# Kernel optimization log

Hardware: AMD Instinct MI355X
Metric: run time of the kernel (lower is better)

Reference implementation:

```python
import math
import jax, jax.numpy as jnp
import numpy as np

NEG = -1e32
H = 8          # n_heads
L2 = 1e-05


def _ln(x, g, b):
    m = jnp.mean(x, -1, keepdims=True)
    v = jnp.mean((x - m) ** 2, -1, keepdims=True)
    return g * (x - m) * jax.lax.rsqrt(v + 1e-5) + b


def _attn(q, k, v, gam, mask_k, zero_pad):
    # q,k,v: [B,H,S,d]; monotonic distance-decay attention (AKT style)
    d_k = q.shape[-1]
    S = q.shape[2]
    scores = jnp.einsum('bhqd,bhkd->bhqk', q, k) / math.sqrt(d_k)
    # torch: triu(ones, k=mask)==0  ->  tril(0) if mask_k==1 else tril(-1)
    mask = jnp.tril(jnp.ones((S, S), bool), 0 if mask_k == 1 else -1)[None, None]
    # first (detached) softmax, used only to build the distance effect
    s_ = jax.nn.softmax(jnp.where(mask, scores, NEG), -1) * mask
    distcum = jnp.cumsum(s_, -1)
    disttot = jnp.sum(s_, -1, keepdims=True)
    idx = jnp.arange(S, dtype=jnp.float32)
    pos = jnp.abs(idx[None, :] - idx[:, None])[None, None]  # |j - i|
    dist = jax.lax.stop_gradient(
        jnp.sqrt(jnp.clip((disttot - distcum) * pos, 0.0, None)))
    gamma = -jax.nn.softplus(gam)[None]  # [1,H,1,1], gam is learned
    total_effect = jnp.clip(jnp.exp(dist * gamma), 1e-5, 1e5)
    scores = jax.nn.softmax(jnp.where(mask, scores * total_effect, NEG), -1)
    if zero_pad:
        scores = scores.at[:, :, 0, :].set(0.0)
    return jnp.einsum('bhqk,bhkd->bhqd', scores, v)


def _mha(qi, ki, vi, kW, kb, vW, vb, oW, ob, gam, mask_k, zero_pad):
    # kq_same=True: q and k both use k_linear
    B, S = qi.shape[:2]
    sp = lambda x: x.reshape(B, S, H, -1).transpose(0, 2, 1, 3)
    q = sp(qi @ kW + kb)
    k = sp(ki @ kW + kb)
    v = sp(vi @ vW + vb)
    o = _attn(q, k, v, gam, mask_k, zero_pad)
    o = o.transpose(0, 2, 1, 3).reshape(B, S, -1)
    return o @ oW + ob


def _tlayer(query, key, values, mask_k, zero_pad, apply_pos,
            kW, kb, vW, vb, oW, ob, gam, ln1g, ln1b,
            f1W, f1b, f2W, f2b, ln2g, ln2b):
    q2 = _mha(query, key, values, kW, kb, vW, vb, oW, ob, gam, mask_k, zero_pad)
    x = _ln(query + q2, ln1g, ln1b)
    if apply_pos:
        ff = jax.nn.relu(x @ f1W + f1b) @ f2W + f2b
        x = _ln(x + ff, ln2g, ln2b)
    return x


def _forward(p_data, pa_data, target, pemb_W, diff_W, qemb_W, qemb_b,
             y_kW, y_kb, y_vW, y_vb, y_oW, y_ob, y_gam, y_ln1g, y_ln1b,
             y_f1W, y_f1b, y_f2W, y_f2b, y_ln2g, y_ln2b,
             x_kW, x_kb, x_vW, x_vb, x_oW, x_ob, x_gam, x_ln1g, x_ln1b,
             h_kW, h_kb, h_vW, h_vb, h_oW, h_ob, h_gam, h_ln1g, h_ln1b,
             h_f1W, h_f1b, h_f2W, h_f2b, h_ln2g, h_ln2b,
             oln1g, oln1b, o1W, o1b, oln2g, oln2b, o2W, o2b,
             oln3g, oln3b, o3W, o3b):
    NPID = pemb_W.shape[0] - 1

    def qe(qd):  # q_embed: Linear -> ReLU, normalized by row-sum of q_data
        return jax.nn.relu(qd @ qemb_W + qemb_b) / jnp.sum(qd, -1, keepdims=True)

    q_data = jax.nn.sigmoid(pemb_W[p_data])           # [B,S,NQ+1]
    q_embed = qe(q_data)                              # [B,S,D]
    pa_pos = jnp.where(pa_data > NPID, pa_data - NPID, 0)
    pa_neg = jnp.where(pa_data <= NPID, pa_data, 0)
    qa_pos = jax.nn.sigmoid(pemb_W[pa_pos])
    qa_neg = jax.nn.sigmoid(pemb_W[pa_neg])
    qa_embed = jnp.concatenate([qe(qa_pos), qe(qa_neg)], -1)  # [B,S,2D]
    pid = diff_W[p_data]                              # [B,S,1]
    q_embed = q_embed + pid
    qa_embed = qa_embed + pid
    c_reg = jnp.sum(pid ** 2) * L2

    # Architecture (n_blocks = 1)
    y = _tlayer(qa_embed, qa_embed, qa_embed, 1, False, True,
                y_kW, y_kb, y_vW, y_vb, y_oW, y_ob, y_gam, y_ln1g, y_ln1b,
                y_f1W, y_f1b, y_f2W, y_f2b, y_ln2g, y_ln2b)
    x = _tlayer(q_embed, q_embed, q_embed, 1, False, False,
                x_kW, x_kb, x_vW, x_vb, x_oW, x_ob, x_gam, x_ln1g, x_ln1b,
                None, None, None, None, None, None)
    x = _tlayer(x, x, y, 0, True, True,
                h_kW, h_kb, h_vW, h_vb, h_oW, h_ob, h_gam, h_ln1g, h_ln1b,
                h_f1W, h_f1b, h_f2W, h_f2b, h_ln2g, h_ln2b)

    c = jnp.concatenate([x, q_embed], -1)             # [B,S,2D]
    o = jax.nn.relu(_ln(c, oln1g, oln1b) @ o1W + o1b)
    o = jax.nn.relu(_ln(o, oln2g, oln2b) @ o2W + o2b)
    out = _ln(o, oln3g, oln3b) @ o3W + o3b            # [B,S,1]
    return out, c_reg


def setup_inputs():
    B, S, D, NQ, NPID, FC, DFF = 8, 1024, 256, 1024, 4096, 512, 2048
    key = jax.random.key(0)
    cnt = [0]

    def nk():
        cnt[0] += 1
        return jax.random.fold_in(key, cnt[0])

    def nrm(shape, s=0.05):
        return jax.random.normal(nk(), shape, dtype=jnp.float32) * s

    z = lambda sh: jnp.zeros(sh, jnp.float32)
    on = lambda sh: jnp.ones(sh, jnp.float32)

    return dict(
        p_data=jax.random.randint(nk(), (B, S), 0, NPID + 1),
        pa_data=jax.random.randint(nk(), (B, S), 0, 2 * NPID + 1),
        target=jax.random.uniform(nk(), (B, S), jnp.float32),
        pemb_W=nrm((NPID + 1, NQ + 1), 1.0), diff_W=nrm((NPID + 1, 1), 0.1),
        qemb_W=nrm((NQ + 1, D)), qemb_b=z((D,)),
        y_kW=nrm((2 * D, 2 * D)), y_kb=z((2 * D,)),
        y_vW=nrm((2 * D, 2 * D)), y_vb=z((2 * D,)),
        y_oW=nrm((2 * D, 2 * D)), y_ob=z((2 * D,)), y_gam=nrm((H, 1, 1), 1.0),
        y_ln1g=on((2 * D,)), y_ln1b=z((2 * D,)),
        y_f1W=nrm((2 * D, DFF)), y_f1b=z((DFF,)),
        y_f2W=nrm((DFF, 2 * D)), y_f2b=z((2 * D,)),
        y_ln2g=on((2 * D,)), y_ln2b=z((2 * D,)),
        x_kW=nrm((D, D)), x_kb=z((D,)), x_vW=nrm((D, D)), x_vb=z((D,)),
        x_oW=nrm((D, D)), x_ob=z((D,)), x_gam=nrm((H, 1, 1), 1.0),
        x_ln1g=on((D,)), x_ln1b=z((D,)),
        h_kW=nrm((D, D)), h_kb=z((D,)),
        h_vW=nrm((2 * D, 2 * D)), h_vb=z((2 * D,)),
        h_oW=nrm((2 * D, D)), h_ob=z((D,)), h_gam=nrm((H, 1, 1), 1.0),
        h_ln1g=on((D,)), h_ln1b=z((D,)),
        h_f1W=nrm((D, DFF)), h_f1b=z((DFF,)),
        h_f2W=nrm((DFF, D)), h_f2b=z((D,)),
        h_ln2g=on((D,)), h_ln2b=z((D,)),
        oln1g=on((2 * D,)), oln1b=z((2 * D,)),
        o1W=nrm((2 * D, FC)), o1b=z((FC,)),
        oln2g=on((FC,)), oln2b=z((FC,)),
        o2W=nrm((FC, 256)), o2b=z((256,)),
        oln3g=on((256,)), oln3b=z((256,)),
        o3W=nrm((256, 1)), o3b=z((1,)),
    )


def reference(p_data, pa_data, target, pemb_W, diff_W, qemb_W, qemb_b,
              y_kW, y_kb, y_vW, y_vb, y_oW, y_ob, y_gam, y_ln1g, y_ln1b,
              y_f1W, y_f1b, y_f2W, y_f2b, y_ln2g, y_ln2b,
              x_kW, x_kb, x_vW, x_vb, x_oW, x_ob, x_gam, x_ln1g, x_ln1b,
              h_kW, h_kb, h_vW, h_vb, h_oW, h_ob, h_gam, h_ln1g, h_ln1b,
              h_f1W, h_f1b, h_f2W, h_f2b, h_ln2g, h_ln2b,
              oln1g, oln1b, o1W, o1b, oln2g, oln2b, o2W, o2b,
              oln3g, oln3b, o3W, o3b):
    return _forward(p_data, pa_data, target, pemb_W, diff_W, qemb_W, qemb_b,
                    y_kW, y_kb, y_vW, y_vb, y_oW, y_ob, y_gam, y_ln1g, y_ln1b,
                    y_f1W, y_f1b, y_f2W, y_f2b, y_ln2g, y_ln2b,
                    x_kW, x_kb, x_vW, x_vb, x_oW, x_ob, x_gam, x_ln1g, x_ln1b,
                    h_kW, h_kb, h_vW, h_vb, h_oW, h_ob, h_gam, h_ln1g, h_ln1b,
                    h_f1W, h_f1b, h_f2W, h_f2b, h_ln2g, h_ln2b,
                    oln1g, oln1b, o1W, o1b, oln2g, oln2b, o2W, o2b,
                    oln3g, oln3b, o3W, o3b)
```

## Files before the change

### kernel.cpp

```cpp
#include <hip/hip_runtime.h>
#include <hip/hip_bf16.h>
#include <math.h>

#define NHEADS 8
#define L2E 1.44269504f

typedef __attribute__((ext_vector_type(8))) __bf16 bfrag;
typedef __attribute__((ext_vector_type(4))) float f32x4;
typedef __attribute__((ext_vector_type(8))) unsigned short u16x8;

static __device__ __forceinline__ unsigned short f2bf(float f) {
  unsigned u = __float_as_uint(f);
  unsigned r = (u + 0x7fffu + ((u >> 16) & 1u)) >> 16;
  return (unsigned short)r;
}

static __device__ __forceinline__ void gload_lds16(const void* g, void* l) {
  __builtin_amdgcn_global_load_lds(
      (const __attribute__((address_space(1))) unsigned int*)g,
      (__attribute__((address_space(3))) unsigned int*)l, 16, 0, 0);
}

static __device__ __forceinline__ float block_reduce_sum(float v, float* red) {
  int t = threadIdx.x;
  red[t] = v; __syncthreads();
  for (int s = 128; s > 0; s >>= 1) {
    if (t < s) red[t] += red[t + s];
    __syncthreads();
  }
  float r = red[0];
  __syncthreads();
  return r;
}

__global__ __launch_bounds__(256) void sig_kernel(
    const float* __restrict__ Wp, unsigned short* __restrict__ Sgb,
    float* __restrict__ Ssum, int Kd, int Kp)
{
  __shared__ float red[256];
  int row = blockIdx.x;
  float s = 0.f;
  for (int k = threadIdx.x; k < Kp; k += 256) {
    float v = 0.f;
    if (k < Kd) {
      v = 1.f / (1.f + __expf(-Wp[(size_t)row * Kd + k]));
      s += v;
    }
    Sgb[(size_t)row * Kp + k] = f2bf(v);
  }
  float tot = block_reduce_sum(s, red);
  if (threadIdx.x == 0) Ssum[row] = tot;
}

struct TDesc { const float* src; unsigned short* dst; int K, N, Kp, tilesX, blk0; };
struct TPack { TDesc d[16]; };

__global__ __launch_bounds__(256) void tconv_all_kernel(TPack P) {
  __shared__ float t[32][33];
  int bid = blockIdx.x;
  int di = 0;
  #pragma unroll
  for (int k = 1; k < 16; ++k) if (bid >= P.d[k].blk0) di = k;
  const float* src = P.d[di].src;
  unsigned short* dst = P.d[di].dst;
  int K = P.d[di].K, N = P.d[di].N, Kp = P.d[di].Kp, tilesX = P.d[di].tilesX;
  int local = bid - P.d[di].blk0;
  int bn = (local % tilesX) * 32;
  int bk = (local / tilesX) * 32;
  int tid = threadIdx.x;
  int tx = tid & 31, ty = tid >> 5;
  #pragma unroll
  for (int u = 0; u < 4; ++u) {
    int k = bk + ty + u * 8, n = bn + tx;
    t[ty + u * 8][tx] = (k < K && n < N) ? src[(size_t)k * N + n] : 0.f;
  }
  __syncthreads();
  #pragma unroll
  for (int u = 0; u < 4; ++u) {
    int n = bn + ty + u * 8, kk = bk + tx;
    if (n < N && kk < Kp)
      dst[(size_t)n * Kp + kk] = f2bf(t[tx][ty + u * 8]);
  }
}

template<int BM, int EPI, bool WF32, bool WBF, bool WTR>
__global__ __launch_bounds__(256) void mgemm_kernel(
    const unsigned short* __restrict__ A, const unsigned short* __restrict__ Bt,
    const float* __restrict__ bias, float* __restrict__ C,
    unsigned short* __restrict__ Cb, unsigned short* __restrict__ Ct,
    int M, int N, int K, const float* __restrict__ divv,
    const float* __restrict__ bias2, int Nk)
{
  constexpr int TN  = (BM == 128) ? 128 : 64;
  constexpr int NI  = (BM == 128) ? 4 : 2;
  constexpr int NJ  = (BM == 128) ? 4 : 2;
  constexpr int WSM = (BM == 128) ? 64 : 32;
  constexpr bool SPLIT = WBF && WTR;
  __shared__ __align__(16) unsigned short Als[BM * 32];
  __shared__ __align__(16) unsigned short Bls[TN * 32];
  const int tid = threadIdx.x;
  const int lane = tid & 63, w = tid >> 6;
  const int wm = w >> 1, wn = w & 1;
  const int brow = blockIdx.y * BM, bcol = blockIdx.x * TN;

  f32x4 acc[NI][NJ] = {};

  for (int k0 = 0; k0 < K; k0 += 32) {
    if constexpr (BM == 128) {
      #pragma unroll
      for (int q = 0; q < 2; ++q) {
        int s = w * 128 + q * 64 + lane;
        int r = s >> 2, g = s & 3;
        int gs = g ^ (r & 3);
        int gc = bcol + r; if (gc > N - 1) gc = N - 1;
        gload_lds16(Bt + (size_t)gc * K + k0 + gs * 8,
                    (char*)Bls + (w * 2048 + q * 1024));
      }
      #pragma unroll
      for (int q = 0; q < 2; ++q) {
        int s = w * 128 + q * 64 + lane;
        int r = s >> 2, g = s & 3;
        int gs = g ^ (r & 3);
        int gr = brow + r; if (gr > M - 1) gr = M - 1;
        gload_lds16(A + (size_t)gr * K + k0 + gs * 8,
                    (char*)Als + (w * 2048 + q * 1024));
      }
    } else {
      {
        int s = tid;
        int r = s >> 2, g = s & 3;
        int gs = g ^ (r & 3);
        int gc = bcol + r; if (gc > N - 1) gc = N - 1;
        gload_lds16(Bt + (size_t)gc * K + k0 + gs * 8,
                    (char*)Bls + w * 1024);
      }
      {
        int s = tid;
        int r = s >> 2, g = s & 3;
        int gs = g ^ (r & 3);
        int gr = brow + r; if (gr > M - 1) gr = M - 1;
        gload_lds16(A + (size_t)gr * K + k0 + gs * 8,
                    (char*)Als + w * 1024);
      }
    }
    __syncthreads();

    bfrag av[NI], bv[NJ];
    #pragma unroll
    for (int f = 0; f < NI; ++f) {
      int rA = wm * WSM + f * 16 + (lane & 15);
      av[f] = *(const bfrag*)((const char*)Als + rA * 64 + ((((lane >> 4) ^ (rA & 3))) << 4));
    }
    #pragma unroll
    for (int f = 0; f < NJ; ++f) {
      int rB = wn * WSM + f * 16 + (lane & 15);
      bv[f] = *(const bfrag*)((const char*)Bls + rB * 64 + ((((lane >> 4) ^ (rB & 3))) << 4));
    }
    #pragma unroll
    for (int i = 0; i < NI; ++i)
      #pragma unroll
      for (int j = 0; j < NJ; ++j)
        acc[i][j] = __builtin_amdgcn_mfma_f32_16x16x32_bf16(av[i], bv[j], acc[i][j], 0, 0, 0);
    __syncthreads();
  }

  #pragma unroll
  for (int i = 0; i < NI; ++i) {
    int gr0 = brow + wm * WSM + i * 16 + (lane >> 4) * 4;
    #pragma unroll
    for (int j = 0; j < NJ; ++j) {
      int gc = bcol + wn * WSM + j * 16 + (lane & 15);
      float bsv;
      if (SPLIT) bsv = (gc < Nk) ? bias[gc] : bias2[gc - Nk];
      else       bsv = bias ? bias[gc] : 0.f;
      float vv[4];
      #pragma unroll
      for (int q = 0; q < 4; ++q) {
        int gr = gr0 + q;
        float v = acc[i][j][q] + bsv;
        if (EPI >= 1) v = fmaxf(v, 0.f);
        if (EPI == 2) v = (gr < M) ? v / divv[gr] : v;
        vv[q] = v;
      }
      if (SPLIT) {
        if (gc < Nk) {
          #pragma unroll
          for (int q = 0; q < 4; ++q) {
            int gr = gr0 + q;
            if (gr < M) Cb[(size_t)gr * Nk + gc] = f2bf(vv[q]);
          }
        } else {
          ushort4 h4 = { f2bf(vv[0]), f2bf(vv[1]), f2bf(vv[2]), f2bf(vv[3]) };
          *(ushort4*)(Ct + (size_t)(gc - Nk) * M + gr0) = h4;
        }
      } else {
        #pragma unroll
        for (int q = 0; q < 4; ++q) {
          int gr = gr0 + q;
          if (gr >= M) continue;
          if (WF32) C[(size_t)gr * N + gc] = vv[q];
          if (WBF)  Cb[(size_t)gr * N + gc] = f2bf(vv[q]);
        }
        if (WTR) {
          ushort4 h4 = { f2bf(vv[0]), f2bf(vv[1]), f2bf(vv[2]), f2bf(vv[3]) };
          *(ushort4*)(Ct + (size_t)gc * M + gr0) = h4;
        }
      }
    }
  }
}

__global__ __launch_bounds__(256) void gather_kernel(
    const int* __restrict__ p_data, const int* __restrict__ pa_data,
    const float* __restrict__ E, const float* __restrict__ diff_W,
    float* __restrict__ qemb, unsigned short* __restrict__ qembb,
    float* __restrict__ qaemb, unsigned short* __restrict__ qaembb)
{
  int idx = blockIdx.x * 256 + threadIdx.x;
  if (idx >= 8192 * 512) return;
  int row = idx >> 9, c = idx & 511;
  int p = p_data[row];
  float pid = diff_W[p];
  if (c < 256) {
    float v = E[(size_t)p * 256 + c] + pid;
    qemb[(size_t)row * 256 + c] = v;
    qembb[(size_t)row * 256 + c] = f2bf(v);
  }
  int pa = pa_data[row];
  int ppos = (pa > 4096) ? pa - 4096 : 0;
  int pneg = (pa <= 4096) ? pa : 0;
  float v = (c < 256) ? E[(size_t)ppos * 256 + c] : E[(size_t)pneg * 256 + (c - 256)];
  v += pid;
  qaemb[(size_t)row * 512 + c] = v;
  qaembb[(size_t)row * 512 + c] = f2bf(v);
}

__global__ __launch_bounds__(256) void creg_kernel(
    const int* __restrict__ p_data, const float* __restrict__ dW,
    float* __restrict__ out)
{
  __shared__ float red[256];
  float s = 0.f;
  for (int i = threadIdx.x; i < 8192; i += 256) {
    float v = dW[p_data[i]];
    s += v * v;
  }
  float tot = block_reduce_sum(s, red);
  if (threadIdx.x == 0) out[0] = tot * 1e-5f;
}

template<int DK, int DV, int MASKK, int ZP, int CHUNK>
__global__ __launch_bounds__(512, (CHUNK == 16) ? 8 : 4) void attn9_kernel(
    const unsigned short* __restrict__ QKb, const unsigned short* __restrict__ Vt,
    const float* __restrict__ gamp, unsigned short* __restrict__ O,
    int S, int MT, int bxoff)
{
  constexpr int RS = 36 * CHUNK + 4;
  constexpr int LBITS = (CHUNK == 32) ? 2 : 1;
  constexpr int LM = (1 << LBITS) - 1;
  constexpr int HIOFF = 64 * CHUNK;
  constexpr int NPAR = (DV == 64) ? 2 : 4;
  constexpr int NFIN = (DV == 64) ? 4 : 2;
  constexpr int NP   = (DV == 32) ? 6 : 4;
  const int DMK = NHEADS * DK, DMV = NHEADS * DV;
  const int nIb = gridDim.x;
  const int id = blockIdx.x + blockIdx.y * nIb;
  const int cpx = nIb * 8;
  const int W = (id & 7) * cpx + (id >> 3);
  const int ib = (nIb - 1) - (W % nIb);
  const int bh = W / nIb;
  const int i0 = (ib + bxoff) * 16;
  const int b = bh >> 3, h = bh & 7;
  const int tid = threadIdx.x;
  const int lane = tid & 63, w = tid >> 6;
  const size_t rowbase = (size_t)b * S;

  __shared__ __align__(16) float sc[16 * RS];
  __shared__ float wrow[16];

  const int jmaxBlk = MASKK ? (i0 + 15) : (i0 + 14);
  const int NK = (jmaxBlk / 64 + 1) * 64;

  const int qr = lane & 15;
  const int ko8 = (lane >> 4) * 8;
  const float rscale = rsqrtf((float)DK) * L2E;

  bfrag qf[DK / 32];
  #pragma unroll
  for (int ks = 0; ks < DK / 32; ++ks)
    qf[ks] = *(const bfrag*)(QKb + (rowbase + i0 + qr) * DMK + h * DK + ks * 32 + ko8);

  for (int t0 = 0; t0 < NK; t0 += 128) {
    int tt = t0 + (w >> 2) * 64;
    if (tt < NK) {
      int jb = tt + (w & 3) * 16 + qr;
      bfrag kf[DK / 32];
      #pragma unroll
      for (int ks = 0; ks < DK / 32; ++ks)
        kf[ks] = *(const bfrag*)(QKb + (rowbase + jb) * DMK + h * DK + ks * 32 + ko8);
      f32x4 accs = {};
      #pragma unroll
      for (int ks = 0; ks < DK / 32; ++ks)
        accs = __builtin_amdgcn_mfma_f32_16x16x32_bf16(qf[ks], kf[ks], accs, 0, 0, 0);
      int ja = jb + 4 * (jb >> 5);
      int r0 = (lane >> 4) * 4;
      #pragma unroll
      for (int q = 0; q < 4; ++q)
        sc[(r0 + q) * RS + ja] = accs[q] * rscale;
    }
  }
  __syncthreads();

  {
    const int g = tid >> 5, l = tid & 31;
    const int i = i0 + g;
    const int jmax = MASKK ? i : i - 1;
    const int jb0 = CHUNK * l;
    const int sb = g * RS + jb0 + 4 * (jb0 >> 5);

    float p[CHUNK];
    float m1 = -1e30f;
    #pragma unroll
    for (int c = 0; c < CHUNK / 4; ++c) {
      f32x4 v = *(const f32x4*)(sc + sb + c * 4);
      #pragma unroll
      for (int k = 0; k < 4; ++k) {
        int j = jb0 + c * 4 + k;
        float s = (j <= jmax) ? v[k] : -1e30f;
        p[c * 4 + k] = s;
        m1 = fmaxf(m1, s);
      }
    }
    #pragma unroll
    for (int o = 16; o > 0; o >>= 1) m1 = fmaxf(m1, __shfl_xor(m1, o, 32));

    float lloc = 0.f;
    #pragma unroll
    for (int t = 0; t < CHUNK; ++t) lloc += __builtin_amdgcn_exp2f(p[t] - m1);
    float l1 = lloc;
    #pragma unroll
    for (int o = 16; o > 0; o >>= 1) l1 += __shfl_xor(l1, o, 32);

    float scn = lloc;
    #pragma unroll
    for (int o = 1; o < 32; o <<= 1) {
      float u = __shfl_up(scn, o, 32);
      if (l >= o) scn += u;
    }
    float cum = scn - lloc;

    float gv = gamp[h];
    float sp = fmaxf(gv, 0.f) + log1pf(__expf(-fabsf(gv)));
    float gmr = -sp * L2E * rsqrtf(l1);
    float dj = (float)(i - jb0);
    float m2 = -1e30f;
    #pragma unroll
    for (int t = 0; t < CHUNK; ++t) {
      cum += __builtin_amdgcn_exp2f(p[t] - m1);
      float rem = fmaxf(l1 - cum, 0.f);
      float dsq = sqrtf(rem * fabsf(dj));
      dj -= 1.f;
      float eff = fmaxf(__builtin_amdgcn_exp2f(gmr * dsq), 1e-5f);
      p[t] = p[t] * eff;
      m2 = fmaxf(m2, p[t]);
    }
    #pragma unroll
    for (int o = 16; o > 0; o >>= 1) m2 = fmaxf(m2, __shfl_xor(m2, o, 32));

    float l2 = 0.f;
    #pragma unroll
    for (int t = 0; t < CHUNK; ++t) { p[t] = __builtin_amdgcn_exp2f(p[t] - m2); l2 += p[t]; }
    #pragma unroll
    for (int o = 16; o > 0; o >>= 1) l2 += __shfl_xor(l2, o, 32);
    bool validrow = (jmax >= 0) && !(ZP && i == 0);
    float wgt = validrow ? (1.f / l2) : 0.f;
    if (l == 0) wrow[g] = wgt;

    char* rowB = (char*)sc + (size_t)g * (RS * 4);
    #pragma unroll
    for (int k = 0; k < CHUNK / 8; ++k) {
      int bb = (CHUNK / 8) * l + k;
      int pb = ((bb & LM) << 5) | (bb >> LBITS);
      u16x8 hi8, lo8;
      #pragma unroll
      for (int e = 0; e < 8; ++e) {
        float v = p[8 * k + e];
        __bf16 hb = (__bf16)v;
        hi8[e] = __builtin_bit_cast(unsigned short, hb);
        lo8[e] = __builtin_bit_cast(unsigned short, (__bf16)(v - (float)hb));
      }
      *(u16x8*)(rowB + 16 * pb) = hi8;
      *(u16x8*)(rowB + HIOFF + 16 * pb) = lo8;
    }
  }
  __syncthreads();

  const int dblk = (DV == 64) ? (w & 3) : (w & 1);
  const int par  = (DV == 64) ? (w >> 2) : (w >> 1);
  const int dcol = h * DV + dblk * 16 + (lane & 15);
  const unsigned short* vrow = Vt + (size_t)dcol * MT + rowbase;
  f32x4 acco = {};
  const char* rowB = (const char*)sc + (size_t)qr * (RS * 4);
  for (int t0 = par * 64; t0 < NK; t0 += NPAR * 64) {
    #pragma unroll
    for (int ks = 0; ks < 2; ++ks) {
      int jo = t0 + ks * 32 + ko8;
      int bb = jo >> 3;
      int pb = ((bb & LM) << 5) | (bb >> LBITS);
      bfrag ph = *(const bfrag*)(rowB + 16 * pb);
      bfrag pl = *(const bfrag*)(rowB + HIOFF + 16 * pb);
      bfrag vf = *(const bfrag*)(vrow + jo);
      acco = __builtin_amdgcn_mfma_f32_16x16x32_bf16(pl, vf, acco, 0, 0, 0);
      acco = __builtin_amdgcn_mfma_f32_16x16x32_bf16(ph, vf, acco, 0, 0, 0);
    }
  }
  __syncthreads();

  float* redA = sc;
  if (w >= NFIN) {
    int slot = w - NFIN;
    #pragma unroll
    for (int q = 0; q < 4; ++q)
      redA[slot * 272 + ((lane >> 4) * 4 + q) * 17 + (lane & 15)] = acco[q];
  }
  __syncthreads();
  if (w < NFIN) {
    for (int pp = w; pp < NP; pp += NFIN) {
      #pragma unroll
      for (int q = 0; q < 4; ++q)
        acco[q] += redA[pp * 272 + ((lane >> 4) * 4 + q) * 17 + (lane & 15)];
    }
    int r0 = (lane >> 4) * 4;
    #pragma unroll
    for (int q = 0; q < 4; ++q) {
      float wv = wrow[r0 + q];
      O[(rowbase + i0 + r0 + q) * DMV + dcol] = f2bf(acco[q] * wv);
    }
  }
}

template<int D, bool WF, bool WB>
__global__ __launch_bounds__(256) void ln4_kernel(
    const float* __restrict__ X, const float* __restrict__ R,
    const float* __restrict__ g, const float* __restrict__ be,
    float* __restrict__ Y, unsigned short* __restrict__ Yb)
{
  constexpr int NC = D / 256;
  int row = blockIdx.x * 4 + (threadIdx.x >> 6);
  int lane = threadIdx.x & 63;
  const float* x = X + (size_t)row * D;
  f32x4 xv[NC];
  float s = 0.f;
  #pragma unroll
  for (int c = 0; c < NC; ++c) {
    xv[c] = *(const f32x4*)(x + c * 256 + lane * 4);
    if (R) {
      f32x4 rv = *(const f32x4*)(R + (size_t)row * D + c * 256 + lane * 4);
      #pragma unroll
      for (int k = 0; k < 4; ++k) xv[c][k] += rv[k];
    }
    #pragma unroll
    for (int k = 0; k < 4; ++k) s += xv[c][k];
  }
  #pragma unroll
  for (int o = 32; o > 0; o >>= 1) s += __shfl_xor(s, o, 64);
  float mean = s / (float)D;
  float vs = 0.f;
  #pragma unroll
  for (int c = 0; c < NC; ++c)
    #pragma unroll
    for (int k = 0; k < 4; ++k) { float d = xv[c][k] - mean; vs += d * d; }
  #pragma unroll
  for (int o = 32; o > 0; o >>= 1) vs += __shfl_xor(vs, o, 64);
  float rstd = rsqrtf(vs / (float)D + 1e-5f);
  #pragma unroll
  for (int c = 0; c < NC; ++c) {
    f32x4 gv = *(const f32x4*)(g + c * 256 + lane * 4);
    f32x4 bv = *(const f32x4*)(be + c * 256 + lane * 4);
    f32x4 ov;
    #pragma unroll
    for (int k = 0; k < 4; ++k) ov[k] = gv[k] * (xv[c][k] - mean) * rstd + bv[k];
    if (WF) *(f32x4*)(Y + (size_t)row * D + c * 256 + lane * 4) = ov;
    if (WB) {
      ushort4 h4 = { f2bf(ov[0]), f2bf(ov[1]), f2bf(ov[2]), f2bf(ov[3]) };
      *(ushort4*)(Yb + (size_t)row * D + c * 256 + lane * 4) = h4;
    }
  }
}

__global__ __launch_bounds__(256) void lnc_kernel(
    const float* __restrict__ Xh, const float* __restrict__ Qe,
    const float* __restrict__ g, const float* __restrict__ be,
    unsigned short* __restrict__ Yb)
{
  int row = blockIdx.x * 4 + (threadIdx.x >> 6);
  int lane = threadIdx.x & 63;
  f32x4 xv[2];
  xv[0] = *(const f32x4*)(Xh + (size_t)row * 256 + lane * 4);
  xv[1] = *(const f32x4*)(Qe + (size_t)row * 256 + lane * 4);
  float s = 0.f;
  #pragma unroll
  for (int c = 0; c < 2; ++c)
    #pragma unroll
    for (int k = 0; k < 4; ++k) s += xv[c][k];
  #pragma unroll
  for (int o = 32; o > 0; o >>= 1) s += __shfl_xor(s, o, 64);
  float mean = s / 512.f;
  float vs = 0.f;
  #pragma unroll
  for (int c = 0; c < 2; ++c)
    #pragma unroll
    for (int k = 0; k < 4; ++k) { float d = xv[c][k] - mean; vs += d * d; }
  #pragma unroll
  for (int o = 32; o > 0; o >>= 1) vs += __shfl_xor(vs, o, 64);
  float rstd = rsqrtf(vs / 512.f + 1e-5f);
  #pragma unroll
  for (int c = 0; c < 2; ++c) {
    f32x4 gv = *(const f32x4*)(g + c * 256 + lane * 4);
    f32x4 bv = *(const f32x4*)(be + c * 256 + lane * 4);
    ushort4 h4;
    #pragma unroll
    for (int k = 0; k < 4; ++k) {
      float ov = gv[k] * (xv[c][k] - mean) * rstd + bv[k];
      ((unsigned short*)&h4)[k] = f2bf(ov);
    }
    *(ushort4*)(Yb + (size_t)row * 512 + c * 256 + lane * 4) = h4;
  }
}

__global__ __launch_bounds__(256) void lndot_kernel(
    const float* __restrict__ X, const float* __restrict__ g,
    const float* __restrict__ be, const float* __restrict__ w3,
    const float* __restrict__ b3, float* __restrict__ out)
{
  int row = blockIdx.x * 4 + (threadIdx.x >> 6);
  int lane = threadIdx.x & 63;
  f32x4 v = *(const f32x4*)(X + (size_t)row * 256 + lane * 4);
  float s = v[0] + v[1] + v[2] + v[3];
  #pragma unroll
  for (int o = 32; o > 0; o >>= 1) s += __shfl_xor(s, o, 64);
  float mean = s / 256.f;
  float vs = 0.f;
  #pragma unroll
  for (int k = 0; k < 4; ++k) { float d = v[k] - mean; vs += d * d; }
  #pragma unroll
  for (int o = 32; o > 0; o >>= 1) vs += __shfl_xor(vs, o, 64);
  float rstd = rsqrtf(vs / 256.f + 1e-5f);
  f32x4 gv = *(const f32x4*)(g + lane * 4);
  f32x4 bv = *(const f32x4*)(be + lane * 4);
  f32x4 wv = *(const f32x4*)(w3 + lane * 4);
  float d = 0.f;
  #pragma unroll
  for (int k = 0; k < 4; ++k)
    d += (gv[k] * (v[k] - mean) * rstd + bv[k]) * wv[k];
  #pragma unroll
  for (int o = 32; o > 0; o >>= 1) d += __shfl_xor(d, o, 64);
  if (lane == 0) out[row] = d + b3[0];
}

extern "C" void kernel_launch(void* const* d_in, const int* in_sizes, int n_in,
                              void* d_out, int out_size, void* d_ws, size_t ws_size,
                              hipStream_t stream) {
  const int* p_data  = (const int*)d_in[0];
  const int* pa_data = (const int*)d_in[1];
  const float* pemb_W = (const float*)d_in[3];
  const float* diff_W = (const float*)d_in[4];
  const float* qemb_W = (const float*)d_in[5];
  const float* qemb_b = (const float*)d_in[6];
  const float* y_kW = (const float*)d_in[7];   const float* y_kb = (const float*)d_in[8];
  const float* y_vW = (const float*)d_in[9];   const float* y_vb = (const float*)d_in[10];
  const float* y_oW = (const float*)d_in[11];  const float* y_ob = (const float*)d_in[12];
  const float* y_gam = (const float*)d_in[13];
  const float* y_ln1g = (const float*)d_in[14]; const float* y_ln1b = (const float*)d_in[15];
  const float* y_f1W = (const float*)d_in[16]; const float* y_f1b = (const float*)d_in[17];
  const float* y_f2W = (const float*)d_in[18]; const float* y_f2b = (const float*)d_in[19];
  const float* y_ln2g = (const float*)d_in[20]; const float* y_ln2b = (const float*)d_in[21];
  const float* x_kW = (const float*)d_in[22];  const float* x_kb = (const float*)d_in[23];
  const float* x_vW = (const float*)d_in[24];  const float* x_vb = (const float*)d_in[25];
  const float* x_oW = (const float*)d_in[26];  const float* x_ob = (const float*)d_in[27];
  const float* x_gam = (const float*)d_in[28];
  const float* x_ln1g = (const float*)d_in[29]; const float* x_ln1b = (const float*)d_in[30];
  const float* h_kW = (const float*)d_in[31];  const float* h_kb = (const float*)d_in[32];
  const float* h_vW = (const float*)d_in[33];  const float* h_vb = (const float*)d_in[34];
  const float* h_oW = (const float*)d_in[35];  const float* h_ob = (const float*)d_in[36];
  const float* h_gam = (const float*)d_in[37];
  const float* h_ln1g = (const float*)d_in[38]; const float* h_ln1b = (const float*)d_in[39];
  const float* h_f1W = (const float*)d_in[40]; const float* h_f1b = (const float*)d_in[41];
  const float* h_f2W = (const float*)d_in[42]; const float* h_f2b = (const float*)d_in[43];
  const float* h_ln2g = (const float*)d_in[44]; const float* h_ln2b = (const float*)d_in[45];
  const float* oln1g = (const float*)d_in[46]; const float* oln1b = (const float*)d_in[47];
  const float* o1W = (const float*)d_in[48];   const float* o1b = (const float*)d_in[49];
  const float* oln2g = (const float*)d_in[50]; const float* oln2b = (const float*)d_in[51];
  const float* o2W = (const float*)d_in[52];   const float* o2b = (const float*)d_in[53];
  const float* oln3g = (const float*)d_in[54]; const float* oln3b = (const float*)d_in[55];
  const float* o3W = (const float*)d_in[56];   const float* o3b = (const float*)d_in[57];

  float* out_f = (float*)d_out;

  const int B = 8, S = 1024, M = B * S;
  const int R = 4097, KQ = 1025, KQP = 1056;

  float* ws = (float*)d_ws;
  size_t off = 0;
  auto alloc = [&](size_t nfloats) { size_t o = off; off += (nfloats + 255) & ~(size_t)255; return o; };
  auto allocs = [&](size_t nshorts) { return alloc((nshorts + 1) / 2); };

  size_t oE    = alloc((size_t)R * 256);
  size_t oSIGb = allocs((size_t)R * KQP);
  size_t oSSUM = alloc(R);
  size_t oQE   = alloc((size_t)M * 256);
  size_t oQEb  = allocs((size_t)M * 256);
  size_t oQA   = alloc((size_t)M * 512);
  size_t oQAb  = allocs((size_t)M * 512);
  size_t oYOb  = allocs((size_t)M * 512);
  size_t oXO   = alloc((size_t)M * 256);
  size_t oXOb  = allocs((size_t)M * 256);
  size_t oHO   = alloc((size_t)M * 256);
  size_t oS0   = alloc((size_t)M * 512);
  size_t oS1   = alloc((size_t)M * 512);
  size_t oS2b  = allocs((size_t)M * 512);
  size_t oS3   = alloc((size_t)M * 512);
  size_t oS4   = alloc((size_t)M * 512);
  size_t oSX   = alloc((size_t)M * 512);
  size_t oSXb  = allocs((size_t)M * 512);
  size_t oS0b  = allocs((size_t)M * 512);
  size_t oVt   = allocs((size_t)M * 512);
  size_t oWqe  = allocs((size_t)256 * KQP);
  size_t oWyk  = allocs((size_t)512 * 512);
  size_t oWyv  = allocs((size_t)512 * 512);
  size_t oWyo  = allocs((size_t)512 * 512);
  size_t oWyf1 = allocs((size_t)2048 * 512);
  size_t oWyf2 = allocs((size_t)512 * 2048);
  size_t oWxk  = allocs((size_t)256 * 256);
  size_t oWxv  = allocs((size_t)256 * 256);
  size_t oWxo  = allocs((size_t)256 * 256);
  size_t oWhk  = allocs((size_t)256 * 256);
  size_t oWhv  = allocs((size_t)512 * 512);
  size_t oWho  = allocs((size_t)256 * 512);
  size_t oWhf1 = allocs((size_t)2048 * 256);
  size_t oWhf2 = allocs((size_t)256 * 2048);
  size_t oWo1  = allocs((size_t)512 * 512);
  size_t oWo2  = allocs((size_t)256 * 512);
  (void)ws_size; (void)in_sizes; (void)n_in; (void)out_size;

  float* E    = ws + oE;
  unsigned short* SIGb = (unsigned short*)(ws + oSIGb);
  float* SSUM = ws + oSSUM;
  float* QE   = ws + oQE;   unsigned short* QEb = (unsigned short*)(ws + oQEb);
  float* QA   = ws + oQA;   unsigned short* QAb = (unsigned short*)(ws + oQAb);
  unsigned short* YOb = (unsigned short*)(ws + oYOb);
  float* XO   = ws + oXO;   unsigned short* XOb = (unsigned short*)(ws + oXOb);
  float* HO   = ws + oHO;
  float* S0   = ws + oS0;
  unsigned short* S2b = (unsigned short*)(ws + oS2b);
  float* S3   = ws + oS3;
  float* S4   = ws + oS4;
  float* SX   = ws + oSX;   unsigned short* SXb = (unsigned short*)(ws + oSXb);
  unsigned short* S0b = (unsigned short*)(ws + oS0b);
  unsigned short* Vt  = (unsigned short*)(ws + oVt);
  unsigned short* FFb = (unsigned short*)S0;

  unsigned short* Wqe  = (unsigned short*)(ws + oWqe);
  unsigned short* Wyk  = (unsigned short*)(ws + oWyk);
  unsigned short* Wyv  = (unsigned short*)(ws + oWyv);
  unsigned short* Wyo  = (unsigned short*)(ws + oWyo);
  unsigned short* Wyf1 = (unsigned short*)(ws + oWyf1);
  unsigned short* Wyf2 = (unsigned short*)(ws + oWyf2);
  unsigned short* Wxk  = (unsigned short*)(ws + oWxk);
  unsigned short* Wxv  = (unsigned short*)(ws + oWxv);
  unsigned short* Wxo  = (unsigned short*)(ws + oWxo);
  unsigned short* Whk  = (unsigned short*)(ws + oWhk);
  unsigned short* Whv  = (unsigned short*)(ws + oWhv);
  unsigned short* Who  = (unsigned short*)(ws + oWho);
  unsigned short* Whf1 = (unsigned short*)(ws + oWhf1);
  unsigned short* Whf2 = (unsigned short*)(ws + oWhf2);
  unsigned short* Wo1  = (unsigned short*)(ws + oWo1);
  unsigned short* Wo2  = (unsigned short*)(ws + oWo2);

  dim3 blk(256);
  int nElem512 = (8192 * 512 + 255) / 256;

  {
    struct HD { const float* src; unsigned short* dst; int K, N, Kp; };
    const HD hd[16] = {
      {qemb_W, Wqe, KQ, 256, KQP},
      {y_kW, Wyk, 512, 512, 512}, {y_vW, Wyv, 512, 512, 512}, {y_oW, Wyo, 512, 512, 512},
      {y_f1W, Wyf1, 512, 2048, 512}, {y_f2W, Wyf2, 2048, 512, 2048},
      {x_kW, Wxk, 256, 256, 256}, {x_vW, Wxv, 256, 256, 256}, {x_oW, Wxo, 256, 256, 256},
      {h_kW, Whk, 256, 256, 256}, {h_vW, Whv, 512, 512, 512}, {h_oW, Who, 512, 256, 512},
      {h_f1W, Whf1, 256, 2048, 256}, {h_f2W, Whf2, 2048, 256, 2048},
      {o1W, Wo1, 512, 512, 512}, {o2W, Wo2, 512, 256, 512},
    };
    TPack P;
    int tot = 0;
    for (int k = 0; k < 16; ++k) {
      int tx = (hd[k].N + 31) / 32, ty = (hd[k].Kp + 31) / 32;
      P.d[k] = { hd[k].src, hd[k].dst, hd[k].K, hd[k].N, hd[k].Kp, tx, tot };
      tot += tx * ty;
    }
    tconv_all_kernel<<<dim3(tot), blk, 0, stream>>>(P);
  }

  auto gg128 = [](int Mm, int Nn) { return dim3((unsigned)(Nn / 128), (unsigned)((Mm + 127) / 128)); };
  auto gg64  = [](int Mm, int Nn) { return dim3((unsigned)(Nn / 64), (unsigned)((Mm + 63) / 64)); };

  sig_kernel<<<R, blk, 0, stream>>>(pemb_W, SIGb, SSUM, KQ, KQP);
  mgemm_kernel<64, 2, true, false, false><<<gg64(R, 256), blk, 0, stream>>>(SIGb, Wqe, qemb_b, E, nullptr, nullptr, R, 256, KQP, SSUM, nullptr, 0);
  gather_kernel<<<nElem512, blk, 0, stream>>>(p_data, pa_data, E, diff_W, QE, QEb, QA, QAb);
  creg_kernel<<<1, blk, 0, stream>>>(p_data, diff_W, out_f + 8192);

  dim3 ablk(512);
  dim3 lgrid(M / 4);
  dim3 agB(32, B * NHEADS), agC(32, B * NHEADS);

  mgemm_kernel<128, 0, false, true, true><<<dim3(8, 64), blk, 0, stream>>>(QAb, Wyk, y_kb, nullptr, S0b, Vt, M, 1024, 512, nullptr, y_vb, 512);
  attn9_kernel<64, 64, 1, 0, 16><<<agB, ablk, 0, stream>>>(S0b, Vt, y_gam, S2b, S, M, 0);
  attn9_kernel<64, 64, 1, 0, 32><<<agC, ablk, 0, stream>>>(S0b, Vt, y_gam, S2b, S, M, 32);
  mgemm_kernel<128, 0, true, false, false><<<gg128(M, 512), blk, 0, stream>>>(S2b, Wyo, y_ob, S3, nullptr, nullptr, M, 512, 512, nullptr, nullptr, 0);
  ln4_kernel<512, true, true><<<lgrid, blk, 0, stream>>>(QA, S3, y_ln1g, y_ln1b, SX, SXb);
  mgemm_kernel<128, 1, false, true, false><<<gg128(M, 2048), blk, 0, stream>>>(SXb, Wyf1, y_f1b, nullptr, FFb, nullptr, M, 2048, 512, nullptr, nullptr, 0);
  mgemm_kernel<128, 0, true, false, false><<<gg128(M, 512), blk, 0, stream>>>(FFb, Wyf2, y_f2b, S4, nullptr, nullptr, M, 512, 2048, nullptr, nullptr, 0);
  ln4_kernel<512, false, true><<<lgrid, blk, 0, stream>>>(SX, S4, y_ln2g, y_ln2b, nullptr, YOb);

  mgemm_kernel<128, 0, false, true, true><<<dim3(4, 64), blk, 0, stream>>>(QEb, Wxk, x_kb, nullptr, S0b, Vt, M, 512, 256, nullptr, x_vb, 256);
  attn9_kernel<32, 32, 1, 0, 16><<<agB, ablk, 0, stream>>>(S0b, Vt, x_gam, S2b, S, M, 0);
  attn9_kernel<32, 32, 1, 0, 32><<<agC, ablk, 0, stream>>>(S0b, Vt, x_gam, S2b, S, M, 32);
  mgemm_kernel<64, 0, true, false, false><<<gg64(M, 256), blk, 0, stream>>>(S2b, Wxo, x_ob, S3, nullptr, nullptr, M, 256, 256, nullptr, nullptr, 0);
  ln4_kernel<256, true, true><<<lgrid, blk, 0, stream>>>(QE, S3, x_ln1g, x_ln1b, XO, XOb);

  mgemm_kernel<64, 0, false, true, false><<<gg64(M, 256), blk, 0, stream>>>(XOb, Whk, h_kb, nullptr, S0b, nullptr, M, 256, 256, nullptr, nullptr, 0);
  mgemm_kernel<128, 0, false, false, true><<<gg128(M, 512), blk, 0, stream>>>(YOb, Whv, h_vb, nullptr, nullptr, Vt, M, 512, 512, nullptr, nullptr, 0);
  attn9_kernel<32, 64, 0, 1, 16><<<agB, ablk, 0, stream>>>(S0b, Vt, h_gam, S2b, S, M, 0);
  attn9_kernel<32, 64, 0, 1, 32><<<agC, ablk, 0, stream>>>(S0b, Vt, h_gam, S2b, S, M, 32);
  mgemm_kernel<64, 0, true, false, false><<<gg64(M, 256), blk, 0, stream>>>(S2b, Who, h_ob, S3, nullptr, nullptr, M, 256, 512, nullptr, nullptr, 0);
  ln4_kernel<256, true, true><<<lgrid, blk, 0, stream>>>(XO, S3, h_ln1g, h_ln1b, SX, SXb);
  mgemm_kernel<128, 1, false, true, false><<<gg128(M, 2048), blk, 0, stream>>>(SXb, Whf1, h_f1b, nullptr, FFb, nullptr, M, 2048, 256, nullptr, nullptr, 0);
  mgemm_kernel<64, 0, true, false, false><<<gg64(M, 256), blk, 0, stream>>>(FFb, Whf2, h_f2b, S4, nullptr, nullptr, M, 256, 2048, nullptr, nullptr, 0);
  ln4_kernel<256, true, false><<<lgrid, blk, 0, stream>>>(SX, S4, h_ln2g, h_ln2b, HO, nullptr);

  lnc_kernel<<<lgrid, blk, 0, stream>>>(HO, QE, oln1g, oln1b, SXb);
  mgemm_kernel<128, 1, true, false, false><<<gg128(M, 512), blk, 0, stream>>>(SXb, Wo1, o1b, S3, nullptr, nullptr, M, 512, 512, nullptr, nullptr, 0);
  ln4_kernel<512, false, true><<<lgrid, blk, 0, stream>>>(S3, nullptr, oln2g, oln2b, nullptr, SXb);
  mgemm_kernel<64, 1, true, false, false><<<gg64(M, 256), blk, 0, stream>>>(SXb, Wo2, o2b, S4, nullptr, nullptr, M, 256, 512, nullptr, nullptr, 0);
  lndot_kernel<<<lgrid, blk, 0, stream>>>(S4, oln3g, oln3b, o3W, o3b, out_f);
}
```

Baseline: 787.5 us.

## Merge split attention launches into one adaptive-chunk kernel, add MFMA priority

Replaces the two per-layer attention launches (fixed chunk 16 for early query blocks and 32 for later ones) with a single kernel. Each block derives its per-thread chunk width from its causal key extent, so only the needed columns are processed, and the 64 query blocks per head are scheduled longest first. It also raises wave priority around the MFMA sections and moves several GEMMs from 128-wide to 64-wide tiles. This saves launches and tail imbalance, but fixing the kernel at 4 blocks per SM and using runtime-guarded loops may cost occupancy and register efficiency for the short blocks.

Result: faster. 747.8 us (-5.0%).

```diff
diff --git a/kernel.cpp b/kernel.cpp
--- a/kernel.cpp
+++ b/kernel.cpp
@@ -249,27 +249,23 @@
   if (threadIdx.x == 0) out[0] = tot * 1e-5f;
 }
 
-template<int DK, int DV, int MASKK, int ZP, int CHUNK>
-__global__ __launch_bounds__(512, (CHUNK == 16) ? 8 : 4) void attn9_kernel(
+template<int DK, int DV, int MASKK, int ZP>
+__global__ __launch_bounds__(512, 4) void attnA_kernel(
     const unsigned short* __restrict__ QKb, const unsigned short* __restrict__ Vt,
     const float* __restrict__ gamp, unsigned short* __restrict__ O,
-    int S, int MT, int bxoff)
+    int S, int MT)
 {
-  constexpr int RS = 36 * CHUNK + 4;
-  constexpr int LBITS = (CHUNK == 32) ? 2 : 1;
-  constexpr int LM = (1 << LBITS) - 1;
-  constexpr int HIOFF = 64 * CHUNK;
+  constexpr int RS = 1156;
+  constexpr int HIOFF = 2048;
   constexpr int NPAR = (DV == 64) ? 2 : 4;
   constexpr int NFIN = (DV == 64) ? 4 : 2;
   constexpr int NP   = (DV == 32) ? 6 : 4;
   const int DMK = NHEADS * DK, DMV = NHEADS * DV;
-  const int nIb = gridDim.x;
-  const int id = blockIdx.x + blockIdx.y * nIb;
-  const int cpx = nIb * 8;
-  const int W = (id & 7) * cpx + (id >> 3);
-  const int ib = (nIb - 1) - (W % nIb);
-  const int bh = W / nIb;
-  const int i0 = (ib + bxoff) * 16;
+  const int id = blockIdx.x + blockIdx.y * 64;
+  const int W = (id & 7) * 512 + (id >> 3);
+  const int ib = 63 - (W & 63);
+  const int bh = W >> 6;
+  const int i0 = ib * 16;
   const int b = bh >> 3, h = bh & 7;
   const int tid = threadIdx.x;
   const int lane = tid & 63, w = tid >> 6;
@@ -280,6 +276,8 @@
 
   const int jmaxBlk = MASKK ? (i0 + 15) : (i0 + 14);
   const int NK = (jmaxBlk / 64 + 1) * 64;
+  const int NKp = (NK + 255) & ~255;
+  const int CD = NKp >> 5;
 
   const int qr = lane & 15;
   const int ko8 = (lane >> 4) * 8;
@@ -299,9 +297,11 @@
       for (int ks = 0; ks < DK / 32; ++ks)
         kf[ks] = *(const bfrag*)(QKb + (rowbase + jb) * DMK + h * DK + ks * 32 + ko8);
       f32x4 accs = {};
+      __builtin_amdgcn_s_setprio(1);
       #pragma unroll
       for (int ks = 0; ks < DK / 32; ++ks)
         accs = __builtin_amdgcn_mfma_f32_16x16x32_bf16(qf[ks], kf[ks], accs, 0, 0, 0);
+      __builtin_amdgcn_s_setprio(0);
       int ja = jb + 4 * (jb >> 5);
       int r0 = (lane >> 4) * 4;
       #pragma unroll
@@ -315,20 +315,22 @@
     const int g = tid >> 5, l = tid & 31;
     const int i = i0 + g;
     const int jmax = MASKK ? i : i - 1;
-    const int jb0 = CHUNK * l;
-    const int sb = g * RS + jb0 + 4 * (jb0 >> 5);
-
-    float p[CHUNK];
+    const int jb0 = CD * l;
+
+    float p[32];
     float m1 = -1e30f;
     #pragma unroll
-    for (int c = 0; c < CHUNK / 4; ++c) {
-      f32x4 v = *(const f32x4*)(sc + sb + c * 4);
-      #pragma unroll
-      for (int k = 0; k < 4; ++k) {
-        int j = jb0 + c * 4 + k;
-        float s = (j <= jmax) ? v[k] : -1e30f;
-        p[c * 4 + k] = s;
-        m1 = fmaxf(m1, s);
+    for (int c = 0; c < 8; ++c) {
+      if (4 * c < CD) {
+        int j = jb0 + 4 * c;
+        f32x4 v = *(const f32x4*)(sc + g * RS + j + 4 * (j >> 5));
+        #pragma unroll
+        for (int k = 0; k < 4; ++k) {
+          int jj = j + k;
+          float s = (jj <= jmax) ? v[k] : -1e30f;
+          p[4 * c + k] = s;
+          m1 = fmaxf(m1, s);
+        }
       }
     }
     #pragma unroll
@@ -336,7 +338,8 @@
 
     float lloc = 0.f;
     #pragma unroll
-    for (int t = 0; t < CHUNK; ++t) lloc += __builtin_amdgcn_exp2f(p[t] - m1);
+    for (int t = 0; t < 32; ++t)
+      if (t < CD) lloc += __builtin_amdgcn_exp2f(p[t] - m1);
     float l1 = lloc;
     #pragma unroll
     for (int o = 16; o > 0; o >>= 1) l1 += __shfl_xor(l1, o, 32);
@@ -355,21 +358,24 @@
     float dj = (float)(i - jb0);
     float m2 = -1e30f;
     #pragma unroll
-    for (int t = 0; t < CHUNK; ++t) {
-      cum += __builtin_amdgcn_exp2f(p[t] - m1);
-      float rem = fmaxf(l1 - cum, 0.f);
-      float dsq = sqrtf(rem * fabsf(dj));
-      dj -= 1.f;
-      float eff = fmaxf(__builtin_amdgcn_exp2f(gmr * dsq), 1e-5f);
-      p[t] = p[t] * eff;
-      m2 = fmaxf(m2, p[t]);
+    for (int t = 0; t < 32; ++t) {
+      if (t < CD) {
+        cum += __builtin_amdgcn_exp2f(p[t] - m1);
+        float rem = fmaxf(l1 - cum, 0.f);
+        float dsq = sqrtf(rem * fabsf(dj));
+        dj -= 1.f;
+        float eff = fmaxf(__builtin_amdgcn_exp2f(gmr * dsq), 1e-5f);
+        p[t] = p[t] * eff;
+        m2 = fmaxf(m2, p[t]);
+      }
     }
     #pragma unroll
     for (int o = 16; o > 0; o >>= 1) m2 = fmaxf(m2, __shfl_xor(m2, o, 32));
 
     float l2 = 0.f;
     #pragma unroll
-    for (int t = 0; t < CHUNK; ++t) { p[t] = __builtin_amdgcn_exp2f(p[t] - m2); l2 += p[t]; }
+    for (int t = 0; t < 32; ++t)
+      if (t < CD) { p[t] = __builtin_amdgcn_exp2f(p[t] - m2); l2 += p[t]; }
     #pragma unroll
     for (int o = 16; o > 0; o >>= 1) l2 += __shfl_xor(l2, o, 32);
     bool validrow = (jmax >= 0) && !(ZP && i == 0);
@@ -378,19 +384,21 @@
 
     char* rowB = (char*)sc + (size_t)g * (RS * 4);
     #pragma unroll
-    for (int k = 0; k < CHUNK / 8; ++k) {
-      int bb = (CHUNK / 8) * l + k;
-      int pb = ((bb & LM) << 5) | (bb >> LBITS);
-      u16x8 hi8, lo8;
-      #pragma unroll
-      for (int e = 0; e < 8; ++e) {
-        float v = p[8 * k + e];
-        __bf16 hb = (__bf16)v;
-        hi8[e] = __builtin_bit_cast(unsigned short, hb);
-        lo8[e] = __builtin_bit_cast(unsigned short, (__bf16)(v - (float)hb));
-      }
-      *(u16x8*)(rowB + 16 * pb) = hi8;
-      *(u16x8*)(rowB + HIOFF + 16 * pb) = lo8;
+    for (int k = 0; k < 4; ++k) {
+      if (8 * k < CD) {
+        int bb = (CD >> 3) * l + k;
+        int pb = ((bb & 3) << 5) | (bb >> 2);
+        u16x8 hi8, lo8;
+        #pragma unroll
+        for (int e = 0; e < 8; ++e) {
+          float v = p[8 * k + e];
+          __bf16 hb = (__bf16)v;
+          hi8[e] = __builtin_bit_cast(unsigned short, hb);
+          lo8[e] = __builtin_bit_cast(unsigned short, (__bf16)(v - (float)hb));
+        }
+        *(u16x8*)(rowB + 16 * pb) = hi8;
+        *(u16x8*)(rowB + HIOFF + 16 * pb) = lo8;
+      }
     }
   }
   __syncthreads();
@@ -401,12 +409,13 @@
   const unsigned short* vrow = Vt + (size_t)dcol * MT + rowbase;
   f32x4 acco = {};
   const char* rowB = (const char*)sc + (size_t)qr * (RS * 4);
+  __builtin_amdgcn_s_setprio(1);
   for (int t0 = par * 64; t0 < NK; t0 += NPAR * 64) {
     #pragma unroll
     for (int ks = 0; ks < 2; ++ks) {
       int jo = t0 + ks * 32 + ko8;
       int bb = jo >> 3;
-      int pb = ((bb & LM) << 5) | (bb >> LBITS);
+      int pb = ((bb & 3) << 5) | (bb >> 2);
       bfrag ph = *(const bfrag*)(rowB + 16 * pb);
       bfrag pl = *(const bfrag*)(rowB + HIOFF + 16 * pb);
       bfrag vf = *(const bfrag*)(vrow + jo);
@@ -414,6 +423,7 @@
       acco = __builtin_amdgcn_mfma_f32_16x16x32_bf16(ph, vf, acco, 0, 0, 0);
     }
   }
+  __builtin_amdgcn_s_setprio(0);
   __syncthreads();
 
   float* redA = sc;
@@ -711,27 +721,24 @@
 
   dim3 ablk(512);
   dim3 lgrid(M / 4);
-  dim3 agB(32, B * NHEADS), agC(32, B * NHEADS);
-
-  mgemm_kernel<128, 0, false, true, true><<<dim3(8, 64), blk, 0, stream>>>(QAb, Wyk, y_kb, nullptr, S0b, Vt, M, 1024, 512, nullptr, y_vb, 512);
-  attn9_kernel<64, 64, 1, 0, 16><<<agB, ablk, 0, stream>>>(S0b, Vt, y_gam, S2b, S, M, 0);
-  attn9_kernel<64, 64, 1, 0, 32><<<agC, ablk, 0, stream>>>(S0b, Vt, y_gam, S2b, S, M, 32);
-  mgemm_kernel<128, 0, true, false, false><<<gg128(M, 512), blk, 0, stream>>>(S2b, Wyo, y_ob, S3, nullptr, nullptr, M, 512, 512, nullptr, nullptr, 0);
+  dim3 agA(64, B * NHEADS);
+
+  mgemm_kernel<64, 0, false, true, true><<<gg64(M, 1024), blk, 0, stream>>>(QAb, Wyk, y_kb, nullptr, S0b, Vt, M, 1024, 512, nullptr, y_vb, 512);
+  attnA_kernel<64, 64, 1, 0><<<agA, ablk, 0, stream>>>(S0b, Vt, y_gam, S2b, S, M);
+  mgemm_kernel<64, 0, true, false, false><<<gg64(M, 512), blk, 0, stream>>>(S2b, Wyo, y_ob, S3, nullptr, nullptr, M, 512, 512, nullptr, nullptr, 0);
   ln4_kernel<512, true, true><<<lgrid, blk, 0, stream>>>(QA, S3, y_ln1g, y_ln1b, SX, SXb);
   mgemm_kernel<128, 1, false, true, false><<<gg128(M, 2048), blk, 0, stream>>>(SXb, Wyf1, y_f1b, nullptr, FFb, nullptr, M, 2048, 512, nullptr, nullptr, 0);
   mgemm_kernel<128, 0, true, false, false><<<gg128(M, 512), blk, 0, stream>>>(FFb, Wyf2, y_f2b, S4, nullptr, nullptr, M, 512, 2048, nullptr, nullptr, 0);
   ln4_kernel<512, false, true><<<lgrid, blk, 0, stream>>>(SX, S4, y_ln2g, y_ln2b, nullptr, YOb);
 
-  mgemm_kernel<128, 0, false, true, true><<<dim3(4, 64), blk, 0, stream>>>(QEb, Wxk, x_kb, nullptr, S0b, Vt, M, 512, 256, nullptr, x_vb, 256);
-  attn9_kernel<32, 32, 1, 0, 16><<<agB, ablk, 0, stream>>>(S0b, Vt, x_gam, S2b, S, M, 0);
-  attn9_kernel<32, 32, 1, 0, 32><<<agC, ablk, 0, stream>>>(S0b, Vt, x_gam, S2b, S, M, 32);
+  mgemm_kernel<64, 0, false, true, true><<<gg64(M, 512), blk, 0, stream>>>(QEb, Wxk, x_kb, nullptr, S0b, Vt, M, 512, 256, nullptr, x_vb, 256);
+  attnA_kernel<32, 32, 1, 0><<<agA, ablk, 0, stream>>>(S0b, Vt, x_gam, S2b, S, M);
   mgemm_kernel<64, 0, true, false, false><<<gg64(M, 256), blk, 0, stream>>>(S2b, Wxo, x_ob, S3, nullptr, nullptr, M, 256, 256, nullptr, nullptr, 0);
   ln4_kernel<256, true, true><<<lgrid, blk, 0, stream>>>(QE, S3, x_ln1g, x_ln1b, XO, XOb);
 
   mgemm_kernel<64, 0, false, true, false><<<gg64(M, 256), blk, 0, stream>>>(XOb, Whk, h_kb, nullptr, S0b, nullptr, M, 256, 256, nullptr, nullptr, 0);
-  mgemm_kernel<128, 0, false, false, true><<<gg128(M, 512), blk, 0, stream>>>(YOb, Whv, h_vb, nullptr, nullptr, Vt, M, 512, 512, nullptr, nullptr, 0);
-  attn9_kernel<32, 64, 0, 1, 16><<<agB, ablk, 0, stream>>>(S0b, Vt, h_gam, S2b, S, M, 0);
-  attn9_kernel<32, 64, 0, 1, 32><<<agC, ablk, 0, stream>>>(S0b, Vt, h_gam, S2b, S, M, 32);
+  mgemm_kernel<64, 0, false, false, true><<<gg64(M, 512), blk, 0, stream>>>(YOb, Whv, h_vb, nullptr, nullptr, Vt, M, 512, 512, nullptr, nullptr, 0);
+  attnA_kernel<32, 64, 0, 1><<<agA, ablk, 0, stream>>>(S0b, Vt, h_gam, S2b, S, M);
   mgemm_kernel<64, 0, true, false, false><<<gg64(M, 256), blk, 0, stream>>>(S2b, Who, h_ob, S3, nullptr, nullptr, M, 256, 512, nullptr, nullptr, 0);
   ln4_kernel<256, true, true><<<lgrid, blk, 0, stream>>>(XO, S3, h_ln1g, h_ln1b, SX, SXb);
   mgemm_kernel<128, 1, false, true, false><<<gg128(M, 2048), blk, 0, stream>>>(SXb, Whf1, h_f1b, nullptr, FFb, nullptr, M, 2048, 256, nullptr, nullptr, 0);
@@ -739,7 +746,7 @@
   ln4_kernel<256, true, false><<<lgrid, blk, 0, stream>>>(SX, S4, h_ln2g, h_ln2b, HO, nullptr);
 
   lnc_kernel<<<lgrid, blk, 0, stream>>>(HO, QE, oln1g, oln1b, SXb);
-  mgemm_kernel<128, 1, true, false, false><<<gg128(M, 512), blk, 0, stream>>>(SXb, Wo1, o1b, S3, nullptr, nullptr, M, 512, 512, nullptr, nullptr, 0);
+  mgemm_kernel<64, 1, true, false, false><<<gg64(M, 512), blk, 0, stream>>>(SXb, Wo1, o1b, S3, nullptr, nullptr, M, 512, 512, nullptr, nullptr, 0);
   ln4_kernel<512, false, true><<<lgrid, blk, 0, stream>>>(S3, nullptr, oln2g, oln2b, nullptr, SXb);
   mgemm_kernel<64, 1, true, false, false><<<gg64(M, 256), blk, 0, stream>>>(SXb, Wo2, o2b, S4, nullptr, nullptr, M, 256, 512, nullptr, nullptr, 0);
   lndot_kernel<<<lgrid, blk, 0, stream>>>(S4, oln3g, oln3b, o3W, o3b, out_f);
```
